# Kernel tuning notes

Measured on AMD Instinct MI355X. Metric: run time of the kernel, lower is better.

Reference implementation:

```python
import jax, jax.numpy as jnp
import numpy as np

S = 16          # spatial_size (adaptive pool output per dim)
EPS = 1e-8      # torch.cosine_similarity eps

def _avg_pool3d(x, s):
    # exact adaptive avg pool when D,H,W divisible by s
    B, C, D, H, W = x.shape
    kd, kh, kw = D // s, H // s, W // s
    x = x.reshape(B, C, s, kd, s, kh, s, kw)
    return x.mean(axis=(3, 5, 7))  # (B, C, s, s, s)

def _flatten_rows(x):
    # (B,C,s,s,s) -> (B*s^3, C), matching view+transpose+flatten
    B, C = x.shape[0], x.shape[1]
    return x.reshape(B, C, -1).transpose(0, 2, 1).reshape(-1, C)

def _cos_sim_matrix(a):
    # pairwise cosine similarity via normalize + GEMM
    norms = jnp.maximum(jnp.linalg.norm(a, axis=-1, keepdims=True), EPS)
    an = a / norms
    return an @ an.T  # (N, N)

def setup_inputs() -> dict:
    key = jax.random.key(0)
    k1, k2 = jax.random.split(key)
    shape = (2, 32, 64, 64, 64)
    p1 = jax.random.normal(k1, shape, dtype=jnp.float32)
    p2 = jax.random.normal(k2, shape, dtype=jnp.float32)
    return {"p1": p1, "p2": p2}

def reference(p1, p2):
    aa = _flatten_rows(_avg_pool3d(p1, S))  # (N, C), N = B*S^3
    bb = _flatten_rows(_avg_pool3d(p2, S))
    sim_a = _cos_sim_matrix(aa)
    sim_b = _cos_sim_matrix(bb)
    return jnp.mean((sim_a - sim_b) ** 2)  # MSELoss
```

## Files before the change

kernel.cpp:

```cpp
#include <hip/hip_runtime.h>
#include <hip/hip_bf16.h>


#define HW   4096
#define DHW  262144
#define NROW 8192
#define C    32

__global__ __launch_bounds__(256) void pool_kernel(
    const float* __restrict__ p1, const float* __restrict__ p2,
    float* __restrict__ Pa, float* __restrict__ Pb)
{
    const int bid = blockIdx.x;
    const int zp  = bid & 15;
    const int c   = (bid >> 4) & 31;
    const int b   = (bid >> 9) & 1;
    const int arr = bid >> 10;

    const float* __restrict__ src = arr ? p2 : p1;
    float* __restrict__ dst       = arr ? Pb : Pa;

    const float4* __restrict__ base = reinterpret_cast<const float4*>(
        src + (size_t)(b * C + c) * DHW + (size_t)(zp * 4) * HW);

    const int tid  = threadIdx.x;
    const int lane = tid & 63;
    const int w    = tid >> 6;

    __shared__ float pool[256];

    #pragma unroll
    for (int j = 0; j < 4; ++j) {
        float s = 0.f;
        #pragma unroll
        for (int dz = 0; dz < 4; ++dz) {
            const int p = j + 4 * dz;
            const float4 v = base[p * 256 + tid];
            s += (v.x + v.y) + (v.z + v.w);
        }
        s += __shfl_xor(s, 16);
        s += __shfl_xor(s, 32);
        const int yp = (4 * j + w) & 15;
        if (lane < 16) pool[yp * 16 + lane] = s * (1.0f / 64.0f);
    }
    __syncthreads();

    const int n = b * 4096 + zp * 256 + tid;
    dst[(size_t)n * C + c] = pool[tid];
}

__global__ __launch_bounds__(256) void gram_kernel(
    const float* __restrict__ Pa, const float* __restrict__ Pb,
    float* __restrict__ G)
{
    const int tid = threadIdx.x;
    const int k  = tid >> 3;
    const int l4 = (tid & 7) * 4;

    __shared__ float As[32 * C];
    __shared__ float Bs[32 * C];

    float gaa[4] = {0.f, 0.f, 0.f, 0.f};
    float gab[4] = {0.f, 0.f, 0.f, 0.f};
    float gbb[4] = {0.f, 0.f, 0.f, 0.f};

    const int row0 = blockIdx.x * 64;
    for (int t = 0; t < 2; ++t) {
        const int r = row0 + t * 32;
        float4 va = reinterpret_cast<const float4*>(Pa + (size_t)r * C)[tid];
        float4 vb = reinterpret_cast<const float4*>(Pb + (size_t)r * C)[tid];

        float ssa = va.x*va.x + va.y*va.y + va.z*va.z + va.w*va.w;
        float ssb = vb.x*vb.x + vb.y*vb.y + vb.z*vb.z + vb.w*vb.w;
        ssa += __shfl_xor(ssa, 1); ssa += __shfl_xor(ssa, 2); ssa += __shfl_xor(ssa, 4);
        ssb += __shfl_xor(ssb, 1); ssb += __shfl_xor(ssb, 2); ssb += __shfl_xor(ssb, 4);
        const float inva = 1.0f / fmaxf(sqrtf(ssa), 1e-8f);
        const float invb = 1.0f / fmaxf(sqrtf(ssb), 1e-8f);
        va.x *= inva; va.y *= inva; va.z *= inva; va.w *= inva;
        vb.x *= invb; vb.y *= invb; vb.z *= invb; vb.w *= invb;

        reinterpret_cast<float4*>(As)[tid] = va;
        reinterpret_cast<float4*>(Bs)[tid] = vb;
        __syncthreads();

        #pragma unroll
        for (int i = 0; i < 32; ++i) {
            const float a_k = As[i * C + k];
            const float b_k = Bs[i * C + k];
            const float4 a_l = *reinterpret_cast<const float4*>(&As[i * C + l4]);
            const float4 b_l = *reinterpret_cast<const float4*>(&Bs[i * C + l4]);
            gaa[0] += a_k * a_l.x;  gaa[1] += a_k * a_l.y;
            gaa[2] += a_k * a_l.z;  gaa[3] += a_k * a_l.w;
            gab[0] += a_k * b_l.x;  gab[1] += a_k * b_l.y;
            gab[2] += a_k * b_l.z;  gab[3] += a_k * b_l.w;
            gbb[0] += b_k * b_l.x;  gbb[1] += b_k * b_l.y;
            gbb[2] += b_k * b_l.z;  gbb[3] += b_k * b_l.w;
        }
        __syncthreads();
    }

    float* Gaa = G;
    float* Gab = G + 1024;
    float* Gbb = G + 2048;
    #pragma unroll
    for (int j = 0; j < 4; ++j) {
        atomicAdd(&Gaa[k * C + l4 + j], gaa[j]);
        atomicAdd(&Gab[k * C + l4 + j], gab[j]);
        atomicAdd(&Gbb[k * C + l4 + j], gbb[j]);
    }
}

__global__ __launch_bounds__(1024) void finalize_kernel(
    const float* __restrict__ G, float* __restrict__ out)
{
    const int t = threadIdx.x;
    const float gaa = G[t];
    const float gab = G[1024 + t];
    const float gbb = G[2048 + t];
    float v = gaa * gaa + gbb * gbb - 2.f * gab * gab;

    __shared__ float red[16];
    #pragma unroll
    for (int off = 32; off > 0; off >>= 1) v += __shfl_down(v, off);
    if ((t & 63) == 0) red[t >> 6] = v;
    __syncthreads();
    if (t < 16) {
        float w = red[t];
        #pragma unroll
        for (int off = 8; off > 0; off >>= 1) w += __shfl_down(w, off);
        if (t == 0) out[0] = w / ((float)NROW * (float)NROW);
    }
}

extern "C" void kernel_launch(void* const* d_in, const int* in_sizes, int n_in,
                              void* d_out, int out_size, void* d_ws, size_t ws_size,
                              hipStream_t stream) {
    const float* p1 = (const float*)d_in[0];
    const float* p2 = (const float*)d_in[1];
    float* out = (float*)d_out;

    float* Pa = (float*)d_ws;
    float* Pb = Pa + (size_t)NROW * C;
    float* G  = Pb + (size_t)NROW * C;

    hipMemsetAsync(G, 0, 3 * 1024 * sizeof(float), stream);

    pool_kernel<<<2048, 256, 0, stream>>>(p1, p2, Pa, Pb);
    gram_kernel<<<128, 256, 0, stream>>>(Pa, Pb, G);
    finalize_kernel<<<1, 1024, 0, stream>>>(G, out);
}
```

Baseline: 167.6 us.

## Fuse memset and finalize into pool/gram kernels with last-block reduction

New measurement: 180.6 us. 1.08x slower.

```diff
diff --git a/kernel.cpp b/kernel.cpp
--- a/kernel.cpp
+++ b/kernel.cpp
@@ -7,11 +7,25 @@
 #define NROW 8192
 #define C    32
 
+__device__ __forceinline__ float4 f4add(const float4 a, const float4 b) {
+    return make_float4(a.x + b.x, a.y + b.y, a.z + b.z, a.w + b.w);
+}
+
 __global__ __launch_bounds__(256) void pool_kernel(
     const float* __restrict__ p1, const float* __restrict__ p2,
-    float* __restrict__ Pa, float* __restrict__ Pb)
+    float* __restrict__ Pa, float* __restrict__ Pb, float* __restrict__ G)
 {
+    const int tid = threadIdx.x;
     const int bid = blockIdx.x;
+
+    if (bid == 0) {
+        #pragma unroll
+        for (int i = 0; i < 13; ++i) {
+            const int idx = tid + i * 256;
+            if (idx < 3136) G[idx] = 0.f;
+        }
+    }
+
     const int zp  = bid & 15;
     const int c   = (bid >> 4) & 31;
     const int b   = (bid >> 9) & 1;
@@ -23,21 +37,24 @@
     const float4* __restrict__ base = reinterpret_cast<const float4*>(
         src + (size_t)(b * C + c) * DHW + (size_t)(zp * 4) * HW);
 
-    const int tid  = threadIdx.x;
     const int lane = tid & 63;
     const int w    = tid >> 6;
 
     __shared__ float pool[256];
 
+    float4 v[8], acc[4];
+    #pragma unroll
+    for (int p = 0; p < 8; ++p) v[p] = base[p * 256 + tid];
+    #pragma unroll
+    for (int j = 0; j < 4; ++j) acc[j] = f4add(v[j], v[j + 4]);
+    #pragma unroll
+    for (int p = 0; p < 8; ++p) v[p] = base[(p + 8) * 256 + tid];
+    #pragma unroll
+    for (int j = 0; j < 4; ++j) acc[j] = f4add(acc[j], f4add(v[j], v[j + 4]));
+
     #pragma unroll
     for (int j = 0; j < 4; ++j) {
-        float s = 0.f;
-        #pragma unroll
-        for (int dz = 0; dz < 4; ++dz) {
-            const int p = j + 4 * dz;
-            const float4 v = base[p * 256 + tid];
-            s += (v.x + v.y) + (v.z + v.w);
-        }
+        float s = (acc[j].x + acc[j].y) + (acc[j].z + acc[j].w);
         s += __shfl_xor(s, 16);
         s += __shfl_xor(s, 32);
         const int yp = (4 * j + w) & 15;
@@ -51,7 +68,8 @@
 
 __global__ __launch_bounds__(256) void gram_kernel(
     const float* __restrict__ Pa, const float* __restrict__ Pb,
-    float* __restrict__ G)
+    float* __restrict__ G,
+    float* __restrict__ out)
 {
     const int tid = threadIdx.x;
     const int k  = tid >> 3;
@@ -60,76 +78,77 @@
     __shared__ float As[32 * C];
     __shared__ float Bs[32 * C];
 
+    const int r = blockIdx.x * 32;
+    float4 va = reinterpret_cast<const float4*>(Pa + (size_t)r * C)[tid];
+    float4 vb = reinterpret_cast<const float4*>(Pb + (size_t)r * C)[tid];
+
+    float ssa = va.x*va.x + va.y*va.y + va.z*va.z + va.w*va.w;
+    float ssb = vb.x*vb.x + vb.y*vb.y + vb.z*vb.z + vb.w*vb.w;
+    ssa += __shfl_xor(ssa, 1); ssa += __shfl_xor(ssa, 2); ssa += __shfl_xor(ssa, 4);
+    ssb += __shfl_xor(ssb, 1); ssb += __shfl_xor(ssb, 2); ssb += __shfl_xor(ssb, 4);
+    const float inva = 1.0f / fmaxf(sqrtf(ssa), 1e-8f);
+    const float invb = 1.0f / fmaxf(sqrtf(ssb), 1e-8f);
+    va.x *= inva; va.y *= inva; va.z *= inva; va.w *= inva;
+    vb.x *= invb; vb.y *= invb; vb.z *= invb; vb.w *= invb;
+
+    reinterpret_cast<float4*>(As)[tid] = va;
+    reinterpret_cast<float4*>(Bs)[tid] = vb;
+    __syncthreads();
+
     float gaa[4] = {0.f, 0.f, 0.f, 0.f};
     float gab[4] = {0.f, 0.f, 0.f, 0.f};
     float gbb[4] = {0.f, 0.f, 0.f, 0.f};
 
-    const int row0 = blockIdx.x * 64;
-    for (int t = 0; t < 2; ++t) {
-        const int r = row0 + t * 32;
-        float4 va = reinterpret_cast<const float4*>(Pa + (size_t)r * C)[tid];
-        float4 vb = reinterpret_cast<const float4*>(Pb + (size_t)r * C)[tid];
-
-        float ssa = va.x*va.x + va.y*va.y + va.z*va.z + va.w*va.w;
-        float ssb = vb.x*vb.x + vb.y*vb.y + vb.z*vb.z + vb.w*vb.w;
-        ssa += __shfl_xor(ssa, 1); ssa += __shfl_xor(ssa, 2); ssa += __shfl_xor(ssa, 4);
-        ssb += __shfl_xor(ssb, 1); ssb += __shfl_xor(ssb, 2); ssb += __shfl_xor(ssb, 4);
-        const float inva = 1.0f / fmaxf(sqrtf(ssa), 1e-8f);
-        const float invb = 1.0f / fmaxf(sqrtf(ssb), 1e-8f);
-        va.x *= inva; va.y *= inva; va.z *= inva; va.w *= inva;
-        vb.x *= invb; vb.y *= invb; vb.z *= invb; vb.w *= invb;
-
-        reinterpret_cast<float4*>(As)[tid] = va;
-        reinterpret_cast<float4*>(Bs)[tid] = vb;
-        __syncthreads();
-
-        #pragma unroll
-        for (int i = 0; i < 32; ++i) {
-            const float a_k = As[i * C + k];
-            const float b_k = Bs[i * C + k];
-            const float4 a_l = *reinterpret_cast<const float4*>(&As[i * C + l4]);
-            const float4 b_l = *reinterpret_cast<const float4*>(&Bs[i * C + l4]);
-            gaa[0] += a_k * a_l.x;  gaa[1] += a_k * a_l.y;
-            gaa[2] += a_k * a_l.z;  gaa[3] += a_k * a_l.w;
-            gab[0] += a_k * b_l.x;  gab[1] += a_k * b_l.y;
-            gab[2] += a_k * b_l.z;  gab[3] += a_k * b_l.w;
-            gbb[0] += b_k * b_l.x;  gbb[1] += b_k * b_l.y;
-            gbb[2] += b_k * b_l.z;  gbb[3] += b_k * b_l.w;
-        }
-        __syncthreads();
+    #pragma unroll
+    for (int i = 0; i < 32; ++i) {
+        const float a_k = As[i * C + k];
+        const float b_k = Bs[i * C + k];
+        const float4 a_l = *reinterpret_cast<const float4*>(&As[i * C + l4]);
+        const float4 b_l = *reinterpret_cast<const float4*>(&Bs[i * C + l4]);
+        gaa[0] += a_k * a_l.x;  gaa[1] += a_k * a_l.y;
+        gaa[2] += a_k * a_l.z;  gaa[3] += a_k * a_l.w;
+        gab[0] += a_k * b_l.x;  gab[1] += a_k * b_l.y;
+        gab[2] += a_k * b_l.z;  gab[3] += a_k * b_l.w;
+        gbb[0] += b_k * b_l.x;  gbb[1] += b_k * b_l.y;
+        gbb[2] += b_k * b_l.z;  gbb[3] += b_k * b_l.w;
     }
 
-    float* Gaa = G;
-    float* Gab = G + 1024;
-    float* Gbb = G + 2048;
     #pragma unroll
     for (int j = 0; j < 4; ++j) {
-        atomicAdd(&Gaa[k * C + l4 + j], gaa[j]);
-        atomicAdd(&Gab[k * C + l4 + j], gab[j]);
-        atomicAdd(&Gbb[k * C + l4 + j], gbb[j]);
+        atomicAdd(&G[k * C + l4 + j],        gaa[j]);
+        atomicAdd(&G[1024 + k * C + l4 + j], gab[j]);
+        atomicAdd(&G[2048 + k * C + l4 + j], gbb[j]);
     }
-}
 
-__global__ __launch_bounds__(1024) void finalize_kernel(
-    const float* __restrict__ G, float* __restrict__ out)
-{
-    const int t = threadIdx.x;
-    const float gaa = G[t];
-    const float gab = G[1024 + t];
-    const float gbb = G[2048 + t];
-    float v = gaa * gaa + gbb * gbb - 2.f * gab * gab;
+    __syncthreads();
+    __shared__ int last_flag;
+    if (tid == 0) {
+        __threadfence();
+        const unsigned t = __hip_atomic_fetch_add(
+            reinterpret_cast<unsigned*>(G + 3072), 1u,
+            __ATOMIC_ACQ_REL, __HIP_MEMORY_SCOPE_AGENT);
+        last_flag = (t == (unsigned)(gridDim.x - 1));
+    }
+    __syncthreads();
+    if (!last_flag) return;
 
-    __shared__ float red[16];
+    float vv = 0.f;
     #pragma unroll
-    for (int off = 32; off > 0; off >>= 1) v += __shfl_down(v, off);
-    if ((t & 63) == 0) red[t >> 6] = v;
+    for (int e0 = 0; e0 < 1024; e0 += 256) {
+        const int e = e0 + tid;
+        const float gA = __hip_atomic_load(G + e,        __ATOMIC_RELAXED, __HIP_MEMORY_SCOPE_AGENT);
+        const float gX = __hip_atomic_load(G + 1024 + e, __ATOMIC_RELAXED, __HIP_MEMORY_SCOPE_AGENT);
+        const float gB = __hip_atomic_load(G + 2048 + e, __ATOMIC_RELAXED, __HIP_MEMORY_SCOPE_AGENT);
+        vv += gA * gA + gB * gB - 2.f * gX * gX;
+    }
+    vv += __shfl_xor(vv, 1);  vv += __shfl_xor(vv, 2);  vv += __shfl_xor(vv, 4);
+    vv += __shfl_xor(vv, 8);  vv += __shfl_xor(vv, 16); vv += __shfl_xor(vv, 32);
+
+    __shared__ float red[4];
+    if ((tid & 63) == 0) red[tid >> 6] = vv;
     __syncthreads();
-    if (t < 16) {
-        float w = red[t];
-        #pragma unroll
-        for (int off = 8; off > 0; off >>= 1) w += __shfl_down(w, off);
-        if (t == 0) out[0] = w / ((float)NROW * (float)NROW);
-    }
+    if (tid == 0)
+        out[0] = (red[0] + red[1] + red[2] + red[3]) * (1.0f / ((float)NROW * (float)NROW));
 }
 
 extern "C" void kernel_launch(void* const* d_in, const int* in_sizes, int n_in,
@@ -143,9 +162,6 @@
     float* Pb = Pa + (size_t)NROW * C;
     float* G  = Pb + (size_t)NROW * C;
 
-    hipMemsetAsync(G, 0, 3 * 1024 * sizeof(float), stream);
-
-    pool_kernel<<<2048, 256, 0, stream>>>(p1, p2, Pa, Pb);
-    gram_kernel<<<128, 256, 0, stream>>>(Pa, Pb, G);
-    finalize_kernel<<<1, 1024, 0, stream>>>(G, out);
+    pool_kernel<<<2048, 256, 0, stream>>>(p1, p2, Pa, Pb, G);
+    gram_kernel<<<256, 256, 0, stream>>>(Pa, Pb, G, out);
 }
```
